# Performance work log

Hardware: AMD Instinct MI355X
Metric: run time of the kernel (lower is better)

## Reference

```python
import jax, jax.numpy as jnp
import numpy as np

N = 100_000   # num destination nodes (adj rows)
M = 100_000   # num source/neighbor nodes (adj cols)
E = 3_200_000 # num edges (avg degree 32)
D_IN = 128
DIM = 128
LEAKY_ALPHA = 0.2  # tf.nn.leaky_relu default


def setup_inputs() -> dict:
    key = jax.random.key(0)
    ks = jax.random.split(key, 7)
    return {
        "self_embedding": jax.random.normal(ks[0], (N, D_IN), jnp.float32),
        "neigh_embedding": jax.random.normal(ks[1], (M, D_IN), jnp.float32),
        "W": jax.random.normal(ks[2], (D_IN, DIM), jnp.float32) / np.sqrt(D_IN).astype(np.float32),
        "w_self": jax.random.normal(ks[3], (DIM, 1), jnp.float32) * 0.1,
        "w_neigh": jax.random.normal(ks[4], (DIM, 1), jnp.float32) * 0.1,
        "edge_row": jax.random.randint(ks[5], (E,), 0, N, jnp.int32),
        "edge_col": jax.random.randint(ks[6], (E,), 0, M, jnp.int32),
    }


def reference(self_embedding, neigh_embedding, W, w_self, w_neigh, edge_row, edge_col):
    # Dense projections (shared weight, no bias)
    from_all = neigh_embedding @ W    # [M, DIM]
    from_self = self_embedding @ W    # [N, DIM]

    # Per-node attention logits
    self_weight = (from_self @ w_self)[:, 0]   # [N]
    all_weight = (from_all @ w_neigh)[:, 0]    # [M]

    # Per-edge score: leaky_relu(self_weight[row] + all_weight[col])
    scores = jax.nn.leaky_relu(self_weight[edge_row] + all_weight[edge_col],
                               negative_slope=LEAKY_ALPHA)  # [E]

    n = self_embedding.shape[0]
    # Sparse (segment) softmax over each row's edges, numerically stable
    row_max = jax.ops.segment_max(scores, edge_row, num_segments=n)
    row_max = jnp.where(jnp.isfinite(row_max), row_max, 0.0)  # guard empty rows
    e = jnp.exp(scores - row_max[edge_row])
    denom = jax.ops.segment_sum(e, edge_row, num_segments=n)
    denom = jnp.where(denom > 0, denom, 1.0)
    alpha = e / denom[edge_row]  # [E]

    # Sparse-dense matmul: output[i] = sum_j alpha_ij * from_all[j]
    agg = jax.ops.segment_sum(alpha[:, None] * from_all[edge_col], edge_row,
                              num_segments=n)  # [N, DIM]

    # renorm=False path: residual with from_self, then activation
    return jax.nn.relu(from_self + agg)
```

## Files before the change

kernel.cpp:

```cpp
#include <hip/hip_runtime.h>
#include <math.h>

#define DIM 128
#define LEAKY 0.2f
#define CAP 80
#define RPB 128
#define NBMAX 1024
#define PART_CHUNK 4096

typedef __attribute__((ext_vector_type(8))) short short8_t;
typedef __attribute__((ext_vector_type(8))) __bf16 bf16x8;
typedef __attribute__((ext_vector_type(4))) float f32x4;

__device__ __forceinline__ unsigned short f32_to_bf16_bits(float x) {
  unsigned u = __float_as_uint(x);
  u += 0x7fffu + ((u >> 16) & 1u);
  return (unsigned short)(u >> 16);
}

__global__ __launch_bounds__(256) void gemm_neigh_q(
    const float* __restrict__ emb, const float* __restrict__ W,
    const float* __restrict__ wvec, unsigned char* __restrict__ fa_i8,
    float* __restrict__ scales, float* __restrict__ wout, int nrows)
{
  __shared__ __align__(16) char smem[34816];
  unsigned short* Wt = (unsigned short*)smem;
  int t = threadIdx.x;
  int lane = t & 63;
  int wid = t >> 6;

  for (int i = t; i < 4096; i += 256) {
    int k = i >> 5;
    int c4 = (i & 31) << 2;
    float4 w4 = *(const float4*)(W + k * 128 + c4);
    Wt[(c4 + 0) * 136 + k] = f32_to_bf16_bits(w4.x);
    Wt[(c4 + 1) * 136 + k] = f32_to_bf16_bits(w4.y);
    Wt[(c4 + 2) * 136 + k] = f32_to_bf16_bits(w4.z);
    Wt[(c4 + 3) * 136 + k] = f32_to_bf16_bits(w4.w);
  }
  __syncthreads();

  int row0 = blockIdx.x * 128 + wid * 32;
  bool active = row0 < nrows;
  int lr = lane & 15;
  int lk = lane >> 4;

  f32x4 acc[2][8];
  if (active) {
    bf16x8 a[2][4];
#pragma unroll
    for (int rf = 0; rf < 2; rf++) {
      int row = row0 + rf * 16 + lr;
      row = min(row, nrows - 1);
      const float* src = emb + (size_t)row * DIM;
#pragma unroll
      for (int ks = 0; ks < 4; ks++) {
        int kb = ks * 32 + lk * 8;
        float4 x = *(const float4*)(src + kb);
        float4 y = *(const float4*)(src + kb + 4);
        union { short8_t s; bf16x8 b; } f;
        f.s[0] = (short)f32_to_bf16_bits(x.x); f.s[1] = (short)f32_to_bf16_bits(x.y);
        f.s[2] = (short)f32_to_bf16_bits(x.z); f.s[3] = (short)f32_to_bf16_bits(x.w);
        f.s[4] = (short)f32_to_bf16_bits(y.x); f.s[5] = (short)f32_to_bf16_bits(y.y);
        f.s[6] = (short)f32_to_bf16_bits(y.z); f.s[7] = (short)f32_to_bf16_bits(y.w);
        a[rf][ks] = f.b;
      }
    }
#pragma unroll
    for (int rf = 0; rf < 2; rf++)
#pragma unroll
      for (int cf = 0; cf < 8; cf++)
        acc[rf][cf] = (f32x4){0.f, 0.f, 0.f, 0.f};
#pragma unroll
    for (int ks = 0; ks < 4; ks++) {
#pragma unroll
      for (int cf = 0; cf < 8; cf++) {
        bf16x8 wf = *(const bf16x8*)(Wt + (cf * 16 + lr) * 136 + ks * 32 + lk * 8);
        acc[0][cf] = __builtin_amdgcn_mfma_f32_16x16x32_bf16(a[0][ks], wf, acc[0][cf], 0, 0, 0);
        acc[1][cf] = __builtin_amdgcn_mfma_f32_16x16x32_bf16(a[1][ks], wf, acc[1][cf], 0, 0, 0);
      }
    }
  }
  __syncthreads();

  unsigned char* Q = (unsigned char*)smem + wid * 4096;
  if (active) {
#pragma unroll
    for (int rf = 0; rf < 2; rf++) {
      float pp[4] = {0.f, 0.f, 0.f, 0.f};
#pragma unroll
      for (int cf = 0; cf < 8; cf++) {
        float wvv = wvec[cf * 16 + lr];
#pragma unroll
        for (int r = 0; r < 4; r++) pp[r] += acc[rf][cf][r] * wvv;
      }
#pragma unroll
      for (int r = 0; r < 4; r++) {
        pp[r] += __shfl_xor(pp[r], 1);
        pp[r] += __shfl_xor(pp[r], 2);
        pp[r] += __shfl_xor(pp[r], 4);
        pp[r] += __shfl_xor(pp[r], 8);
      }
      float m[4];
#pragma unroll
      for (int r = 0; r < 4; r++) {
        float mm = 0.f;
#pragma unroll
        for (int cf = 0; cf < 8; cf++) mm = fmaxf(mm, fabsf(acc[rf][cf][r]));
        mm = fmaxf(mm, __shfl_xor(mm, 1));
        mm = fmaxf(mm, __shfl_xor(mm, 2));
        mm = fmaxf(mm, __shfl_xor(mm, 4));
        mm = fmaxf(mm, __shfl_xor(mm, 8));
        m[r] = mm;
      }
#pragma unroll
      for (int r = 0; r < 4; r++) {
        int rl = rf * 16 + lk * 4 + r;
        int row = row0 + rl;
        float inv = m[r] > 0.f ? 127.f / m[r] : 0.f;
        if (row < nrows && lr == 0) {
          wout[row] = pp[r];
          scales[row] = m[r] * (1.f / 127.f);
        }
#pragma unroll
        for (int cf = 0; cf < 8; cf++) {
          int q = (int)__builtin_rintf(acc[rf][cf][r] * inv) + 128;
          Q[rl * 128 + cf * 16 + lr] = (unsigned char)(q & 0xff);
        }
      }
    }
  }
  __syncthreads();

  if (active) {
    unsigned char* dstb = fa_i8 + (size_t)row0 * DIM;
    int nbytes = min(32, nrows - row0) * DIM;
    for (int i = lane * 16; i < 4096; i += 1024) {
      if (i < nbytes)
        *(uint4*)(dstb + i) = *(const uint4*)(Q + i);
    }
  }
}

__global__ __launch_bounds__(256) void gemm_self_f32(
    const float* __restrict__ emb, const float* __restrict__ W,
    const float* __restrict__ wvec, float* __restrict__ out,
    float* __restrict__ wout, int nrows)
{
  __shared__ unsigned short Wt[128 * 136];
  int t = threadIdx.x;
  int lane = t & 63;
  int wid = t >> 6;

  for (int i = t; i < 4096; i += 256) {
    int k = i >> 5;
    int c4 = (i & 31) << 2;
    float4 w4 = *(const float4*)(W + k * 128 + c4);
    Wt[(c4 + 0) * 136 + k] = f32_to_bf16_bits(w4.x);
    Wt[(c4 + 1) * 136 + k] = f32_to_bf16_bits(w4.y);
    Wt[(c4 + 2) * 136 + k] = f32_to_bf16_bits(w4.z);
    Wt[(c4 + 3) * 136 + k] = f32_to_bf16_bits(w4.w);
  }
  __syncthreads();

  int row0 = blockIdx.x * 128 + wid * 32;
  if (row0 >= nrows) return;

  int lr = lane & 15;
  int lk = lane >> 4;

  bf16x8 a[2][4];
#pragma unroll
  for (int rf = 0; rf < 2; rf++) {
    int row = row0 + rf * 16 + lr;
    row = min(row, nrows - 1);
    const float* src = emb + (size_t)row * DIM;
#pragma unroll
    for (int ks = 0; ks < 4; ks++) {
      int kb = ks * 32 + lk * 8;
      float4 x = *(const float4*)(src + kb);
      float4 y = *(const float4*)(src + kb + 4);
      union { short8_t s; bf16x8 b; } f;
      f.s[0] = (short)f32_to_bf16_bits(x.x); f.s[1] = (short)f32_to_bf16_bits(x.y);
      f.s[2] = (short)f32_to_bf16_bits(x.z); f.s[3] = (short)f32_to_bf16_bits(x.w);
      f.s[4] = (short)f32_to_bf16_bits(y.x); f.s[5] = (short)f32_to_bf16_bits(y.y);
      f.s[6] = (short)f32_to_bf16_bits(y.z); f.s[7] = (short)f32_to_bf16_bits(y.w);
      a[rf][ks] = f.b;
    }
  }

  f32x4 acc[2][8];
#pragma unroll
  for (int rf = 0; rf < 2; rf++)
#pragma unroll
    for (int cf = 0; cf < 8; cf++)
      acc[rf][cf] = (f32x4){0.f, 0.f, 0.f, 0.f};

#pragma unroll
  for (int ks = 0; ks < 4; ks++) {
#pragma unroll
    for (int cf = 0; cf < 8; cf++) {
      bf16x8 wf = *(const bf16x8*)(Wt + (cf * 16 + lr) * 136 + ks * 32 + lk * 8);
      acc[0][cf] = __builtin_amdgcn_mfma_f32_16x16x32_bf16(a[0][ks], wf, acc[0][cf], 0, 0, 0);
      acc[1][cf] = __builtin_amdgcn_mfma_f32_16x16x32_bf16(a[1][ks], wf, acc[1][cf], 0, 0, 0);
    }
  }

#pragma unroll
  for (int rf = 0; rf < 2; rf++) {
    float pp[4] = {0.f, 0.f, 0.f, 0.f};
#pragma unroll
    for (int cf = 0; cf < 8; cf++) {
      float wvv = wvec[cf * 16 + lr];
#pragma unroll
      for (int r = 0; r < 4; r++) pp[r] += acc[rf][cf][r] * wvv;
    }
#pragma unroll
    for (int r = 0; r < 4; r++) {
      pp[r] += __shfl_xor(pp[r], 1);
      pp[r] += __shfl_xor(pp[r], 2);
      pp[r] += __shfl_xor(pp[r], 4);
      pp[r] += __shfl_xor(pp[r], 8);
    }
#pragma unroll
    for (int r = 0; r < 4; r++) {
      int row = row0 + rf * 16 + lk * 4 + r;
      if (row < nrows) {
        if (lr == 0) wout[row] = pp[r];
#pragma unroll
        for (int cf = 0; cf < 8; cf++)
          out[(size_t)row * DIM + cf * 16 + lr] = acc[rf][cf][r];
      }
    }
  }
}

__global__ __launch_bounds__(256) void partition_edges(
    const int* __restrict__ erow, const int* __restrict__ ecol,
    unsigned* __restrict__ streams, int capB, int* __restrict__ gcur,
    int E, int nb)
{
  __shared__ int cnt[NBMAX];
  __shared__ int base_[NBMAX];
  __shared__ int pos[NBMAX];
  int t = threadIdx.x;
  for (int i = t; i < nb; i += 256) { cnt[i] = 0; pos[i] = 0; }
  __syncthreads();

  int e0 = blockIdx.x * PART_CHUNK + t * 16;
  int rows[16], cols[16];
#pragma unroll
  for (int q = 0; q < 4; q++) {
    int e = e0 + q * 4;
    if (e + 3 < E) {
      *(int4*)(rows + q * 4) = *(const int4*)(erow + e);
      *(int4*)(cols + q * 4) = *(const int4*)(ecol + e);
    } else {
#pragma unroll
      for (int j = 0; j < 4; j++) {
        rows[q * 4 + j] = (e + j < E) ? erow[e + j] : -1;
        cols[q * 4 + j] = (e + j < E) ? ecol[e + j] : 0;
      }
    }
  }
#pragma unroll
  for (int j = 0; j < 16; j++)
    if (rows[j] >= 0) atomicAdd(&cnt[rows[j] >> 7], 1);
  __syncthreads();
  for (int i = t; i < nb; i += 256)
    base_[i] = cnt[i] ? atomicAdd(gcur + i, cnt[i]) : 0;
  __syncthreads();
#pragma unroll
  for (int j = 0; j < 16; j++) {
    if (rows[j] >= 0) {
      int b = rows[j] >> 7;
      int idx = base_[b] + atomicAdd(&pos[b], 1);
      if (idx < capB)
        streams[(size_t)b * capB + idx] =
            (unsigned)cols[j] | ((unsigned)(rows[j] & (RPB - 1)) << 20);
    }
  }
}

__global__ __launch_bounds__(256) void bucket_scatter(
    const unsigned* __restrict__ streams, int capB,
    const int* __restrict__ gcur, unsigned* __restrict__ perm,
    int* __restrict__ deg, int N)
{
  __shared__ __align__(16) unsigned slots[RPB * CAP];
  __shared__ int cnt[RPB];
  int b = blockIdx.x;
  int t = threadIdx.x;
  for (int i = t; i < RPB; i += 256) cnt[i] = 0;
  __syncthreads();

  int n = min(gcur[b], capB);
  const unsigned* s = streams + (size_t)b * capB;
  for (int i = t; i < n; i += 256) {
    unsigned v = s[i];
    int rl = v >> 20;
    int p = atomicAdd(&cnt[rl], 1);
    if (p < CAP) slots[rl * CAP + p] = v & 0xFFFFFu;
  }
  __syncthreads();

  int row0 = b * RPB;
  unsigned* dst = perm + (size_t)row0 * CAP;
  const int W4 = CAP / 4;
  for (int i = t; i < RPB * W4; i += 256) {
    int rl = i / W4, w = i - rl * W4;
    if (w * 4 < min(cnt[rl], CAP))
      *(uint4*)(dst + rl * CAP + w * 4) = *(const uint4*)(slots + rl * CAP + w * 4);
  }
  for (int i = t; i < RPB; i += 256) {
    int row = row0 + i;
    if (row < N) deg[row] = min(cnt[i], CAP);
  }
}

__global__ __launch_bounds__(256) void aggregate_kernel(
    const unsigned char* __restrict__ fa_i8,
    const float* __restrict__ scales,
    const unsigned* __restrict__ perm, const int* __restrict__ deg_arr,
    const float* __restrict__ sw, const float* __restrict__ aw,
    float* __restrict__ out, int n)
{
  int wid = threadIdx.x >> 6;
  int lane = threadIdx.x & 63;
  int row = blockIdx.x * 4 + wid;
  if (row >= n) return;
  int deg = deg_arr[row];
  size_t base = (size_t)row * CAP;

  int g  = lane >> 3;
  int sl = lane & 7;

  size_t o = (size_t)row * DIM + sl * 16;
  float4 rr0, rr1, rr2, rr3;
  if (g == 0) {
    rr0 = *(const float4*)(out + o);
    rr1 = *(const float4*)(out + o + 4);
    rr2 = *(const float4*)(out + o + 8);
    rr3 = *(const float4*)(out + o + 12);
  }

  float acc[16];
#pragma unroll
  for (int k = 0; k < 16; k++) acc[k] = 0.f;
  float dsum = 0.f, Bl = 0.f;
  float swr = sw[row];

  for (int bb = 0; bb < deg; bb += 64) {
    int nact = min(64, deg - bb);
    int c = 0; float e = 0.f, a = 0.f;
    if (lane < nact) {
      c = (int)perm[base + bb + lane];
      float v = swr + aw[c];
      v = v > 0.f ? v : LEAKY * v;
      e = __expf(v);
      a = e * scales[c];
    }
    dsum += e;

    for (int half = 0; half < 2; half++) {
      if (half * 32 >= nact) break;
#pragma unroll
      for (int jj = 0; jj < 4; jj++) {
        int eidx = half * 32 + (jj << 3) + g;
        float aj = __shfl(a, eidx);
        int   cj = __shfl(c, eidx);
        uint4 u = *(const uint4*)(fa_i8 + (size_t)cj * DIM + sl * 16);
        Bl += aj;
        acc[0]  += aj * (float)( u.x        & 0xffu);
        acc[1]  += aj * (float)((u.x >> 8 ) & 0xffu);
        acc[2]  += aj * (float)((u.x >> 16) & 0xffu);
        acc[3]  += aj * (float)( u.x >> 24);
        acc[4]  += aj * (float)( u.y        & 0xffu);
        acc[5]  += aj * (float)((u.y >> 8 ) & 0xffu);
        acc[6]  += aj * (float)((u.y >> 16) & 0xffu);
        acc[7]  += aj * (float)( u.y >> 24);
        acc[8]  += aj * (float)( u.z        & 0xffu);
        acc[9]  += aj * (float)((u.z >> 8 ) & 0xffu);
        acc[10] += aj * (float)((u.z >> 16) & 0xffu);
        acc[11] += aj * (float)( u.z >> 24);
        acc[12] += aj * (float)( u.w        & 0xffu);
        acc[13] += aj * (float)((u.w >> 8 ) & 0xffu);
        acc[14] += aj * (float)((u.w >> 16) & 0xffu);
        acc[15] += aj * (float)( u.w >> 24);
      }
    }
  }

#pragma unroll
  for (int off = 32; off >= 1; off >>= 1) dsum += __shfl_xor(dsum, off);
  Bl += __shfl_xor(Bl, 8); Bl += __shfl_xor(Bl, 16); Bl += __shfl_xor(Bl, 32);
#pragma unroll
  for (int k = 0; k < 16; k++) {
    acc[k] += __shfl_xor(acc[k], 8);
    acc[k] += __shfl_xor(acc[k], 16);
    acc[k] += __shfl_xor(acc[k], 32);
  }
  float B = -128.f * Bl;
  float inv = dsum > 0.f ? 1.f / dsum : 1.f;

  if (g == 0) {
    float r[16] = {rr0.x, rr0.y, rr0.z, rr0.w, rr1.x, rr1.y, rr1.z, rr1.w,
                   rr2.x, rr2.y, rr2.z, rr2.w, rr3.x, rr3.y, rr3.z, rr3.w};
#pragma unroll
    for (int k = 0; k < 16; k++) {
      float x = r[k] + (acc[k] + B) * inv;
      r[k] = x > 0.f ? x : 0.f;
    }
    *(float4*)(out + o)      = make_float4(r[0],  r[1],  r[2],  r[3]);
    *(float4*)(out + o + 4)  = make_float4(r[4],  r[5],  r[6],  r[7]);
    *(float4*)(out + o + 8)  = make_float4(r[8],  r[9],  r[10], r[11]);
    *(float4*)(out + o + 12) = make_float4(r[12], r[13], r[14], r[15]);
  }
}

extern "C" void kernel_launch(void* const* d_in, const int* in_sizes, int n_in,
                              void* d_out, int out_size, void* d_ws, size_t ws_size,
                              hipStream_t stream)
{
  const float* self_emb  = (const float*)d_in[0];
  const float* neigh_emb = (const float*)d_in[1];
  const float* W         = (const float*)d_in[2];
  const float* w_self    = (const float*)d_in[3];
  const float* w_neigh   = (const float*)d_in[4];
  const int*   erow      = (const int*)d_in[5];
  const int*   ecol      = (const int*)d_in[6];

  const int N = in_sizes[0] / DIM;
  const int M = in_sizes[1] / DIM;
  const int E = in_sizes[5];

  float* out = (float*)d_out;

  char* ws = (char*)d_ws;
  size_t off = 0;
  auto alloc = [&](size_t bytes) -> char* {
    char* p = ws + off;
    off += (bytes + 255) & ~(size_t)255;
    return p;
  };
  unsigned char* fa_i8  = (unsigned char*)alloc((size_t)M * DIM);
  float* scales = (float*)alloc((size_t)M * sizeof(float));
  float* all_w  = (float*)alloc((size_t)M * sizeof(float));
  float* self_w = (float*)alloc((size_t)N * sizeof(float));
  int*   deg    = (int*)alloc((size_t)N * sizeof(int));
  int*   gcur   = (int*)alloc(NBMAX * sizeof(int));
  unsigned* perm = (unsigned*)alloc((size_t)N * CAP * sizeof(unsigned));

  const int nb = (N + RPB - 1) / RPB;
  const int capB = E / nb + 1024;
  unsigned* streams = (unsigned*)alloc((size_t)nb * capB * sizeof(unsigned));

  hipMemsetAsync(gcur, 0, nb * sizeof(int), stream);

  gemm_neigh_q<<<(M + 127) / 128, 256, 0, stream>>>(neigh_emb, W, w_neigh,
                                                    fa_i8, scales, all_w, M);

  gemm_self_f32<<<(N + 127) / 128, 256, 0, stream>>>(self_emb, W, w_self,
                                                     out, self_w, N);

  int pblocks = (E + PART_CHUNK - 1) / PART_CHUNK;
  partition_edges<<<pblocks, 256, 0, stream>>>(erow, ecol, streams, capB, gcur, E, nb);

  bucket_scatter<<<nb, 256, 0, stream>>>(streams, capB, gcur, perm, deg, N);

  aggregate_kernel<<<(N + 3) / 4, 256, 0, stream>>>(fa_i8, scales, perm, deg,
                                                    self_w, all_w, out, N);
}
```

Baseline: 242.8 us.

## Move edge softmax weights into bucket scatter and pack bf16 weight with column

Edge scores, exponentials, per-row denominators, and the scale-multiplied weights are now computed in the bucket scatter kernel. Each weight is packed as 15 bf16 bits above a 17-bit column index in the perm array. The aggregate kernel then skips the aw/scales gathers, the exp, and the dsum reduction, and reads a precomputed inverse denominator. This trades per-edge random gathers in the hot aggregate loop for extra work and shared-memory atomics in the scatter. It also loses precision on the weight (bf16 with the sign bit dropped) and assumes column indices fit in 17 bits.

Result: slower. 267.0 us (+10.0%).

```diff
diff --git a/kernel.cpp b/kernel.cpp
--- a/kernel.cpp
+++ b/kernel.cpp
@@ -284,14 +284,24 @@
 
 __global__ __launch_bounds__(256) void bucket_scatter(
     const unsigned* __restrict__ streams, int capB,
-    const int* __restrict__ gcur, unsigned* __restrict__ perm,
-    int* __restrict__ deg, int N)
+    const int* __restrict__ gcur,
+    const float* __restrict__ sw, const float* __restrict__ aw,
+    const float* __restrict__ scales,
+    unsigned* __restrict__ perm, int* __restrict__ deg,
+    float* __restrict__ invd, int N)
 {
   __shared__ __align__(16) unsigned slots[RPB * CAP];
   __shared__ int cnt[RPB];
+  __shared__ float dsum[RPB];
+  __shared__ float sw_l[RPB];
   int b = blockIdx.x;
   int t = threadIdx.x;
-  for (int i = t; i < RPB; i += 256) cnt[i] = 0;
+  int row0 = b * RPB;
+  if (t < RPB) {
+    cnt[t] = 0; dsum[t] = 0.f;
+    int row = row0 + t;
+    sw_l[t] = (row < N) ? sw[row] : 0.f;
+  }
   __syncthreads();
 
   int n = min(gcur[b], capB);
@@ -304,32 +314,44 @@
   }
   __syncthreads();
 
-  int row0 = b * RPB;
   unsigned* dst = perm + (size_t)row0 * CAP;
-  const int W4 = CAP / 4;
-  for (int i = t; i < RPB * W4; i += 256) {
-    int rl = i / W4, w = i - rl * W4;
-    if (w * 4 < min(cnt[rl], CAP))
-      *(uint4*)(dst + rl * CAP + w * 4) = *(const uint4*)(slots + rl * CAP + w * 4);
-  }
-  for (int i = t; i < RPB; i += 256) {
-    int row = row0 + i;
-    if (row < N) deg[row] = min(cnt[i], CAP);
+  for (int i = t; i < RPB * CAP; i += 256) {
+    int rl = i / CAP;
+    int p = i - rl * CAP;
+    if (p < min(cnt[rl], CAP)) {
+      unsigned col = slots[i];
+      float sc = sw_l[rl] + aw[col];
+      sc = sc > 0.f ? sc : LEAKY * sc;
+      float e = __expf(sc);
+      atomicAdd(&dsum[rl], e);
+      float a = e * scales[col];
+      unsigned eb = f32_to_bf16_bits(a);
+      dst[i] = col | (eb << 17);
+    }
+  }
+  __syncthreads();
+
+  if (t < RPB) {
+    int row = row0 + t;
+    if (row < N) {
+      deg[row] = min(cnt[t], CAP);
+      float d = dsum[t];
+      invd[row] = d > 0.f ? 1.f / d : 1.f;
+    }
   }
 }
 
 __global__ __launch_bounds__(256) void aggregate_kernel(
     const unsigned char* __restrict__ fa_i8,
-    const float* __restrict__ scales,
     const unsigned* __restrict__ perm, const int* __restrict__ deg_arr,
-    const float* __restrict__ sw, const float* __restrict__ aw,
-    float* __restrict__ out, int n)
+    const float* __restrict__ invd, float* __restrict__ out, int n)
 {
   int wid = threadIdx.x >> 6;
   int lane = threadIdx.x & 63;
   int row = blockIdx.x * 4 + wid;
   if (row >= n) return;
   int deg = deg_arr[row];
+  float inv = invd[row];
   size_t base = (size_t)row * CAP;
 
   int g  = lane >> 3;
@@ -347,28 +369,21 @@
   float acc[16];
 #pragma unroll
   for (int k = 0; k < 16; k++) acc[k] = 0.f;
-  float dsum = 0.f, Bl = 0.f;
-  float swr = sw[row];
+  float Bl = 0.f;
 
   for (int bb = 0; bb < deg; bb += 64) {
     int nact = min(64, deg - bb);
-    int c = 0; float e = 0.f, a = 0.f;
-    if (lane < nact) {
-      c = (int)perm[base + bb + lane];
-      float v = swr + aw[c];
-      v = v > 0.f ? v : LEAKY * v;
-      e = __expf(v);
-      a = e * scales[c];
-    }
-    dsum += e;
+    unsigned v = 0;
+    if (lane < nact) v = perm[base + bb + lane];
 
     for (int half = 0; half < 2; half++) {
       if (half * 32 >= nact) break;
 #pragma unroll
       for (int jj = 0; jj < 4; jj++) {
         int eidx = half * 32 + (jj << 3) + g;
-        float aj = __shfl(a, eidx);
-        int   cj = __shfl(c, eidx);
+        unsigned vj = __shfl(v, eidx);
+        int   cj = vj & 0x1FFFFu;
+        float aj = __uint_as_float((vj >> 17) << 16);
         uint4 u = *(const uint4*)(fa_i8 + (size_t)cj * DIM + sl * 16);
         Bl += aj;
         acc[0]  += aj * (float)( u.x        & 0xffu);
@@ -391,8 +406,6 @@
     }
   }
 
-#pragma unroll
-  for (int off = 32; off >= 1; off >>= 1) dsum += __shfl_xor(dsum, off);
   Bl += __shfl_xor(Bl, 8); Bl += __shfl_xor(Bl, 16); Bl += __shfl_xor(Bl, 32);
 #pragma unroll
   for (int k = 0; k < 16; k++) {
@@ -401,7 +414,6 @@
     acc[k] += __shfl_xor(acc[k], 32);
   }
   float B = -128.f * Bl;
-  float inv = dsum > 0.f ? 1.f / dsum : 1.f;
 
   if (g == 0) {
     float r[16] = {rr0.x, rr0.y, rr0.z, rr0.w, rr1.x, rr1.y, rr1.z, rr1.w,
@@ -448,6 +460,7 @@
   float* all_w  = (float*)alloc((size_t)M * sizeof(float));
   float* self_w = (float*)alloc((size_t)N * sizeof(float));
   int*   deg    = (int*)alloc((size_t)N * sizeof(int));
+  float* invd   = (float*)alloc((size_t)N * sizeof(float));
   int*   gcur   = (int*)alloc(NBMAX * sizeof(int));
   unsigned* perm = (unsigned*)alloc((size_t)N * CAP * sizeof(unsigned));
 
@@ -466,8 +479,8 @@
   int pblocks = (E + PART_CHUNK - 1) / PART_CHUNK;
   partition_edges<<<pblocks, 256, 0, stream>>>(erow, ecol, streams, capB, gcur, E, nb);
 
-  bucket_scatter<<<nb, 256, 0, stream>>>(streams, capB, gcur, perm, deg, N);
-
-  aggregate_kernel<<<(N + 3) / 4, 256, 0, stream>>>(fa_i8, scales, perm, deg,
-                                                    self_w, all_w, out, N);
-}
+  bucket_scatter<<<nb, 256, 0, stream>>>(streams, capB, gcur, self_w, all_w,
+                                         scales, perm, deg, invd, N);
+
+  aggregate_kernel<<<(N + 3) / 4, 256, 0, stream>>>(fa_i8, perm, deg, invd, out, N);
+}
```
